# Optimization experiments

Measured on AMD Instinct MI355X. Metric: run time of the kernel, lower is better.

## Reference

```python
import jax, jax.numpy as jnp
import numpy as np

B, S_SRC, S_TGT, H, V = 32, 128, 64, 300, 32000


def setup_inputs() -> dict:
    key = jax.random.key(0)
    ks = jax.random.split(key, 16)

    def n(k, shape, scale=0.05):
        return jax.random.normal(k, shape, dtype=jnp.float32) * scale

    return {
        "x": jax.random.randint(ks[0], (B, S_SRC), 0, V),
        "y": jax.random.randint(ks[1], (B, S_TGT), 0, V),
        "h0": jax.random.normal(ks[2], (B, H), dtype=jnp.float32),  # encoder initNormState (L=1 squeezed)
        "EN": n(ks[3], (V, H)),
        "ZH": n(ks[4], (V, H)),
        "enc_Wih": n(ks[5], (H, H)),
        "enc_Whh": n(ks[6], (H, H)),
        "enc_bih": n(ks[7], (H,)),
        "enc_bhh": n(ks[8], (H,)),
        "dec_Wih": n(ks[9], (H, H)),
        "dec_Whh": n(ks[10], (H, H)),
        "dec_bih": n(ks[11], (H,)),
        "dec_bhh": n(ks[12], (H,)),
        "W_out": n(ks[13], (V, H)),
        "b_out": n(ks[14], (V,)),
    }


def reference(x, y, h0, EN, ZH, enc_Wih, enc_Whh, enc_bih, enc_bhh,
              dec_Wih, dec_Whh, dec_bih, dec_bhh, W_out, b_out):
    # ---- encoder: 1-layer tanh RNN over source embeddings ----
    xe = EN[x]  # [B, S_src, H]

    def enc_step(h, xt):  # xt: [B, H]
        h = jnp.tanh(xt @ enc_Wih.T + enc_bih + h @ enc_Whh.T + enc_bhh)
        return h, None

    c, _ = jax.lax.scan(enc_step, h0, jnp.swapaxes(xe, 0, 1))  # c: [B, H] final hidden

    # ---- decoder: original loop always feeds encoder state c (never the updated
    # hidden) to the RNNCell; with teacher forcing (start_TF_rate=1.0) every step
    # uses y_in[t], so all T steps vectorize into one batched computation. ----
    ye = ZH[y]  # [B, T, H]
    dec_state_term = c @ dec_Whh.T + dec_bhh  # [B, H], shared across all steps
    h_dec = jnp.tanh(ye @ dec_Wih.T + dec_bih + dec_state_term[:, None, :])  # [B, T, H]
    out = h_dec @ W_out.T + b_out  # [B, T, V]
    return out
```

## Files before the change

### kernel.cpp

```cpp
#include <hip/hip_runtime.h>
#include <hip/hip_bf16.h>
#include <stdint.h>

#define BB 32
#define S_SRC 128
#define S_TGT 64
#define H 300
#define VV 32000
#define M_ROWS (BB * S_TGT)
#define KP 320

#define MEGA_T 640
#define ENC_BLK 32
#define HDEC_BLK 128
#define WCVT_BLK 96

typedef __attribute__((ext_vector_type(8))) __bf16 bf16x8;
typedef __attribute__((ext_vector_type(4))) float f32x4;
typedef __attribute__((ext_vector_type(4))) unsigned short u16x4;
typedef __attribute__((ext_vector_type(2))) __fp16 f16x2;

#if defined(__has_builtin)
#if __has_builtin(__builtin_amdgcn_fdot2)
#define HAVE_FDOT2 1
#endif
#endif

__device__ inline unsigned short f2bf(float f) {
    union { float f; unsigned u; } v; v.f = f;
    unsigned r = (v.u + 0x7FFF + ((v.u >> 16) & 1)) >> 16;
    return (unsigned short)r;
}

__device__ __forceinline__ float ftanh(float x) {
    float e = __builtin_amdgcn_exp2f(x * 2.8853900817779268f);
    return 1.0f - 2.0f * __builtin_amdgcn_rcpf(e + 1.0f);
}

__device__ __forceinline__ float fdot2(f16x2 a, f16x2 b, float c) {
#ifdef HAVE_FDOT2
    return __builtin_amdgcn_fdot2(a, b, c, false);
#else
    return c + (float)a.x * (float)b.x + (float)a.y * (float)b.y;
#endif
}

__device__ __forceinline__ void gl_lds16(const void* g, void* l) {
    __builtin_amdgcn_global_load_lds(
        (const __attribute__((address_space(1))) void*)g,
        (__attribute__((address_space(3))) void*)l, 16, 0, 0);
}

__global__ void transpose4(const float* W0, const float* W1, const float* W2,
                           const float* W3, float* dst) {
    const float* srcs[4] = {W0, W1, W2, W3};
    const float* src = srcs[blockIdx.z];
    float* d = dst + (size_t)blockIdx.z * (H * H);
    __shared__ float tile[32][33];
    int j0 = blockIdx.y * 32, k0 = blockIdx.x * 32;
    for (int r = threadIdx.y; r < 32; r += blockDim.y) {
        int j = j0 + r, k = k0 + threadIdx.x;
        tile[r][threadIdx.x] = (j < H && k < H) ? src[(size_t)j * H + k] : 0.f;
    }
    __syncthreads();
    for (int r = threadIdx.y; r < 32; r += blockDim.y) {
        int k = k0 + r, j = j0 + threadIdx.x;
        if (k < H && j < H) d[(size_t)k * H + j] = tile[threadIdx.x][r];
    }
}

#define RPB 8
__global__ __launch_bounds__(192) void pproj(const int* __restrict__ x,
                                             const float* __restrict__ EN,
                                             const float* __restrict__ WihT,
                                             const float* __restrict__ bih,
                                             const float* __restrict__ bhh,
                                             float* __restrict__ P) {
    __shared__ float xe[RPB][H];
    int m0 = blockIdx.x * RPB;
    int tid = threadIdx.x;
    for (int r = 0; r < RPB; ++r) {
        int idx = x[m0 + r];
        for (int c = tid; c < H; c += 192) xe[r][c] = EN[(size_t)idx * H + c];
    }
    __syncthreads();
    if (tid < 150) {
        int j = tid * 2;
        float a0[RPB], a1[RPB];
#pragma unroll
        for (int r = 0; r < RPB; ++r) { a0[r] = 0.f; a1[r] = 0.f; }
        const float* wp = WihT + j;
        for (int k = 0; k < H; ++k) {
            float2 w = *reinterpret_cast<const float2*>(wp + (size_t)k * H);
#pragma unroll
            for (int r = 0; r < RPB; ++r) {
                float xv = xe[r][k];
                a0[r] += xv * w.x; a1[r] += xv * w.y;
            }
        }
        float b0 = bih[j] + bhh[j], b1 = bih[j + 1] + bhh[j + 1];
#pragma unroll
        for (int r = 0; r < RPB; ++r) {
            P[(size_t)(m0 + r) * H + j]     = a0[r] + b0;
            P[(size_t)(m0 + r) * H + j + 1] = a1[r] + b1;
        }
    }
}

__global__ __launch_bounds__(MEGA_T) void mega(
    const float* __restrict__ h0, const float* __restrict__ P,
    const float* __restrict__ Whh, float* __restrict__ c,
    const int* __restrict__ yv, const float* __restrict__ ZH,
    const float* __restrict__ WihT_d, const float* __restrict__ bih_d,
    float* __restrict__ t1,
    const float* __restrict__ W, unsigned short* __restrict__ Wb) {
    __shared__ union {
        __fp16 hb[2][304];
        float  ye[16][304];
    } L;
    int blk = blockIdx.x, tid = threadIdx.x;

    if (blk < ENC_BLK) {
        int b = blk;
        bool act = tid < 600;
        int j = tid >> 1, half = tid & 1;
        f16x2 w[76];
        if (act) {
            const float* wr = Whh + (size_t)j * H + half * 150;
#pragma unroll
            for (int i = 0; i < 75; ++i) {
                float2 f = *reinterpret_cast<const float2*>(wr + 2 * i);
                w[i] = __builtin_amdgcn_cvt_pkrtz(f.x, f.y);
            }
            w[75] = __builtin_amdgcn_cvt_pkrtz(0.f, 0.f);
        }
        if (act && half == 0) {
            int pos = j < 150 ? j : j + 2;
            L.hb[0][pos] = (__fp16)h0[(size_t)b * H + j];
        }
        if (tid >= 600 && tid < 608) {
            int pi = tid - 600, bufi = pi >> 2, q = pi & 3;
            int idx = (q < 2) ? (150 + q) : (302 + (q - 2));
            L.hb[bufi][idx] = (__fp16)0.f;
        }
        __syncthreads();

        const float* Pb = P + (size_t)b * S_SRC * H;
        int cur = 0;
        for (int t = 0; t < S_SRC; ++t) {
            float pv = 0.f;
            if (act && half == 0) pv = Pb[(size_t)t * H + j];
            float tot = 0.f;
            if (act) {
                float a0 = 0.f, a1 = 0.f, a2 = 0.f, a3 = 0.f;
                const uint2* hp =
                    reinterpret_cast<const uint2*>(&L.hb[cur][half * 152]);
#pragma unroll
                for (int i = 0; i < 38; i += 2) {
                    uint2 qa = hp[i];
                    uint2 qb = hp[i + 1];
                    a0 = fdot2(w[2 * i],     __builtin_bit_cast(f16x2, qa.x), a0);
                    a1 = fdot2(w[2 * i + 1], __builtin_bit_cast(f16x2, qa.y), a1);
                    a2 = fdot2(w[2 * i + 2], __builtin_bit_cast(f16x2, qb.x), a2);
                    a3 = fdot2(w[2 * i + 3], __builtin_bit_cast(f16x2, qb.y), a3);
                }
                float a = (a0 + a1) + (a2 + a3);
                tot = a + __shfl_xor(a, 1, 64);
                if (half == 0) {
                    float hv = ftanh(tot + pv);
                    int pos = j < 150 ? j : j + 2;
                    L.hb[cur ^ 1][pos] = (__fp16)hv;
                }
            }
            __syncthreads();
            cur ^= 1;
        }
        if (act && half == 0) {
            int pos = j < 150 ? j : j + 2;
            c[(size_t)b * H + j] = (float)L.hb[cur][pos];
        }
    } else if (blk < ENC_BLK + HDEC_BLK) {
        int bi = blk - ENC_BLK;
        int m0 = bi * 16;
        for (int i = tid; i < 16 * 304; i += MEGA_T) {
            int r = i / 304, cc = i - r * 304;
            L.ye[r][cc] = (cc < H) ? ZH[(size_t)yv[m0 + r] * H + cc] : 0.f;
        }
        __syncthreads();
        if (tid < 600) {
            int rg = tid / 150, jp = tid - rg * 150, j0 = 2 * jp;
            float a[4][2] = {};
            const float* wp = WihT_d + j0;
            for (int k = 0; k < H; k += 2) {
                float2 wa = *reinterpret_cast<const float2*>(wp + (size_t)k * H);
                float2 wb = *reinterpret_cast<const float2*>(wp + (size_t)(k + 1) * H);
#pragma unroll
                for (int r = 0; r < 4; ++r) {
                    float2 x = *reinterpret_cast<const float2*>(&L.ye[rg * 4 + r][k]);
                    a[r][0] += x.x * wa.x + x.y * wb.x;
                    a[r][1] += x.x * wa.y + x.y * wb.y;
                }
            }
            float b0 = bih_d[j0], b1 = bih_d[j0 + 1];
#pragma unroll
            for (int r = 0; r < 4; ++r) {
                *reinterpret_cast<float2*>(&t1[(size_t)(m0 + rg * 4 + r) * 304 + j0]) =
                    make_float2(a[r][0] + b0, a[r][1] + b1);
            }
        }
    } else if (Wb != nullptr) {
        for (int id = (blk - (ENC_BLK + HDEC_BLK)) * MEGA_T + tid; id < VV * 80;
             id += WCVT_BLK * MEGA_T) {
            int row = id / 80, cq = id - row * 80;
            int k = cq * 4;
            u16x4 o;
            if (k < H) {
                float4 f = *reinterpret_cast<const float4*>(W + (size_t)row * H + k);
                o[0] = f2bf(f.x); o[1] = f2bf(f.y); o[2] = f2bf(f.z); o[3] = f2bf(f.w);
            } else {
                o[0] = 0; o[1] = 0; o[2] = 0; o[3] = 0;
            }
            *reinterpret_cast<u16x4*>(Wb + (size_t)row * KP + k) = o;
        }
    }
}

__global__ __launch_bounds__(192) void sdec(const float* __restrict__ c,
                                            const float* __restrict__ WhhT_d,
                                            const float* __restrict__ bhh_d,
                                            float* __restrict__ s2) {
    __shared__ float cl[H];
    int b = blockIdx.x, tid = threadIdx.x;
    for (int k = tid; k < H; k += 192) cl[k] = c[(size_t)b * H + k];
    __syncthreads();
    if (tid < 150) {
        int j = tid * 2;
        float a0 = 0.f, a1 = 0.f;
        const float* wp = WhhT_d + j;
        for (int k = 0; k < H; ++k) {
            float2 w = *reinterpret_cast<const float2*>(wp + (size_t)k * H);
            a0 += cl[k] * w.x; a1 += cl[k] * w.y;
        }
        s2[(size_t)b * H + j]     = a0 + bhh_d[j];
        s2[(size_t)b * H + j + 1] = a1 + bhh_d[j + 1];
    }
}

__global__ __launch_bounds__(256) void hdec_fin(const float* __restrict__ t1,
                                                const float* __restrict__ s2,
                                                unsigned short* __restrict__ hdec) {
    int blk = blockIdx.x, tid = threadIdx.x;
    for (int i = tid; i < 8 * KP; i += 256) {
        int r = i / KP, j = i - r * KP;
        int m = blk * 8 + r, b = m >> 6;
        unsigned short v = 0;
        if (j < H)
            v = f2bf(ftanh(t1[(size_t)m * 304 + j] + s2[(size_t)b * H + j]));
        hdec[(size_t)m * KP + j] = v;
    }
}

__global__ __launch_bounds__(256) void gemm2(const unsigned short* __restrict__ A,
                                             const unsigned short* __restrict__ Wb,
                                             const float* __restrict__ bout,
                                             float* __restrict__ out) {
    __shared__ unsigned short Al[2][128 * 64];
    __shared__ unsigned short Blds[2][128 * 64];
    int tid = threadIdx.x;
    int lane = tid & 63, wv = tid >> 6;
    int wm = wv >> 1, wn = wv & 1;

    int orig = blockIdx.x;
    int wg = (orig & 7) * 500 + (orig >> 3);
    int mi = wg & 15, ni = wg >> 4;
    int m0 = mi * 128, n0 = ni * 128;

    int rowb = tid >> 3;
    int sc2 = (tid & 7) ^ (rowb & 7);

    f32x4 acc[4][4];
    f32x4 zero = {0.f, 0.f, 0.f, 0.f};
#pragma unroll
    for (int i = 0; i < 4; ++i)
#pragma unroll
        for (int j = 0; j < 4; ++j) acc[i][j] = zero;

#pragma unroll
    for (int i = 0; i < 4; ++i) {
        int row = i * 32 + rowb;
        gl_lds16(A + (size_t)(m0 + row) * KP + sc2 * 8, &Al[0][(i * 256 + tid) * 8]);
    }
#pragma unroll
    for (int i = 0; i < 4; ++i) {
        int row = i * 32 + rowb;
        gl_lds16(Wb + (size_t)(n0 + row) * KP + sc2 * 8, &Blds[0][(i * 256 + tid) * 8]);
    }

    for (int t = 0; t < 5; ++t) {
        __syncthreads();
        int buf = t & 1;
        if (t < 4) {
            int k0 = (t + 1) * 64, nb = buf ^ 1;
#pragma unroll
            for (int i = 0; i < 4; ++i) {
                int row = i * 32 + rowb;
                gl_lds16(A + (size_t)(m0 + row) * KP + k0 + sc2 * 8,
                         &Al[nb][(i * 256 + tid) * 8]);
            }
#pragma unroll
            for (int i = 0; i < 4; ++i) {
                int row = i * 32 + rowb;
                gl_lds16(Wb + (size_t)(n0 + row) * KP + k0 + sc2 * 8,
                         &Blds[nb][(i * 256 + tid) * 8]);
            }
        }
        bf16x8 af[2][4], bb[2][4];
#pragma unroll
        for (int ks = 0; ks < 2; ++ks)
#pragma unroll
            for (int i = 0; i < 4; ++i) {
                int ch = (ks * 4 + (lane >> 4)) ^ (lane & 7);
                int rowA = wm * 64 + i * 16 + (lane & 15);
                af[ks][i] = *reinterpret_cast<const bf16x8*>(&Al[buf][rowA * 64 + ch * 8]);
                int rowB = wn * 64 + i * 16 + (lane & 15);
                bb[ks][i] = *reinterpret_cast<const bf16x8*>(&Blds[buf][rowB * 64 + ch * 8]);
            }
#pragma unroll
        for (int ks = 0; ks < 2; ++ks)
#pragma unroll
            for (int i = 0; i < 4; ++i)
#pragma unroll
                for (int j = 0; j < 4; ++j)
                    acc[i][j] = __builtin_amdgcn_mfma_f32_16x16x32_bf16(
                        af[ks][i], bb[ks][j], acc[i][j], 0, 0, 0);
    }

#pragma unroll
    for (int j = 0; j < 4; ++j) {
        int col = n0 + wn * 64 + j * 16 + (lane & 15);
        float bo = bout[col];
#pragma unroll
        for (int i = 0; i < 4; ++i) {
            int rb = m0 + wm * 64 + i * 16 + (lane >> 4) * 4;
            f32x4 v = acc[i][j];
#pragma unroll
            for (int r = 0; r < 4; ++r)
                out[(size_t)(rb + r) * VV + col] = v[r] + bo;
        }
    }
}

#define LDSW 40
__global__ __launch_bounds__(256) void gemm_out(const unsigned short* __restrict__ A,
                                                const float* __restrict__ W,
                                                const float* __restrict__ bout,
                                                float* __restrict__ out) {
    __shared__ __align__(16) unsigned short Alds[128 * LDSW];
    __shared__ __align__(16) unsigned short Bl[128 * LDSW];
    int tid = threadIdx.x;
    int lane = tid & 63, wv = tid >> 6;
    int wm = wv >> 1, wn = wv & 1;
    int m0 = blockIdx.y * 128, n0 = blockIdx.x * 128;

    f32x4 acc[4][4];
    f32x4 zero = {0.f, 0.f, 0.f, 0.f};
#pragma unroll
    for (int i = 0; i < 4; ++i)
#pragma unroll
        for (int jj = 0; jj < 4; ++jj) acc[i][jj] = zero;

    for (int k0 = 0; k0 < KP; k0 += 32) {
#pragma unroll
        for (int s = 0; s < 2; ++s) {
            int slot = tid + s * 256;
            int row = slot >> 2, c16 = slot & 3;
            uint4 v = *reinterpret_cast<const uint4*>(
                &A[(size_t)(m0 + row) * KP + k0 + c16 * 8]);
            *reinterpret_cast<uint4*>(&Alds[row * LDSW + c16 * 8]) = v;
        }
#pragma unroll
        for (int s = 0; s < 2; ++s) {
            int slot = tid + s * 256;
            int row = slot >> 2, c8 = slot & 3;
            int k = k0 + c8 * 8;
            __align__(16) unsigned short tmp[8];
            if (k + 7 < H) {
                const float* src = &W[(size_t)(n0 + row) * H + k];
                float4 f0 = *reinterpret_cast<const float4*>(src);
                float4 f1 = *reinterpret_cast<const float4*>(src + 4);
                tmp[0] = f2bf(f0.x); tmp[1] = f2bf(f0.y);
                tmp[2] = f2bf(f0.z); tmp[3] = f2bf(f0.w);
                tmp[4] = f2bf(f1.x); tmp[5] = f2bf(f1.y);
                tmp[6] = f2bf(f1.z); tmp[7] = f2bf(f1.w);
            } else {
#pragma unroll
                for (int jv = 0; jv < 8; ++jv) {
                    int kk = k + jv;
                    tmp[jv] = (kk < H) ? f2bf(W[(size_t)(n0 + row) * H + kk])
                                       : (unsigned short)0;
                }
            }
            *reinterpret_cast<uint4*>(&Bl[row * LDSW + c8 * 8]) =
                *reinterpret_cast<const uint4*>(tmp);
        }
        __syncthreads();
        bf16x8 af[4], bfm[4];
#pragma unroll
        for (int i = 0; i < 4; ++i) {
            int row = wm * 64 + i * 16 + (lane & 15);
            af[i] = *reinterpret_cast<const bf16x8*>(&Alds[row * LDSW + (lane >> 4) * 8]);
        }
#pragma unroll
        for (int i = 0; i < 4; ++i) {
            int row = wn * 64 + i * 16 + (lane & 15);
            bfm[i] = *reinterpret_cast<const bf16x8*>(&Bl[row * LDSW + (lane >> 4) * 8]);
        }
#pragma unroll
        for (int i = 0; i < 4; ++i)
#pragma unroll
            for (int jj = 0; jj < 4; ++jj)
                acc[i][jj] = __builtin_amdgcn_mfma_f32_16x16x32_bf16(
                    af[i], bfm[jj], acc[i][jj], 0, 0, 0);
        __syncthreads();
    }
#pragma unroll
    for (int jj = 0; jj < 4; ++jj) {
        int col = n0 + wn * 64 + jj * 16 + (lane & 15);
        float bo = bout[col];
#pragma unroll
        for (int i = 0; i < 4; ++i) {
            int rb = m0 + wm * 64 + i * 16 + (lane >> 4) * 4;
            f32x4 v = acc[i][jj];
#pragma unroll
            for (int r = 0; r < 4; ++r)
                out[(size_t)(rb + r) * VV + col] = v[r] + bo;
        }
    }
}

extern "C" void kernel_launch(void* const* d_in, const int* in_sizes, int n_in,
                              void* d_out, int out_size, void* d_ws, size_t ws_size,
                              hipStream_t stream) {
    const int*   x       = (const int*)d_in[0];
    const int*   y       = (const int*)d_in[1];
    const float* h0      = (const float*)d_in[2];
    const float* EN      = (const float*)d_in[3];
    const float* ZH      = (const float*)d_in[4];
    const float* enc_Wih = (const float*)d_in[5];
    const float* enc_Whh = (const float*)d_in[6];
    const float* enc_bih = (const float*)d_in[7];
    const float* enc_bhh = (const float*)d_in[8];
    const float* dec_Wih = (const float*)d_in[9];
    const float* dec_Whh = (const float*)d_in[10];
    const float* dec_bih = (const float*)d_in[11];
    const float* dec_bhh = (const float*)d_in[12];
    const float* W_out   = (const float*)d_in[13];
    const float* b_out   = (const float*)d_in[14];
    float* out = (float*)d_out;
    char* base = (char*)d_ws;

    const size_t needA = 23307520, needB = 2827520;
    bool bigws = (ws_size >= needA);
    if (!bigws && ws_size < needB) return;

    float* WT = (float*)base;
    float *c_, *s2_;
    unsigned short *hdec, *Wb = nullptr;
    if (bigws) {
        Wb   = (unsigned short*)(base + 1440000);
        c_   = (float*)(base + 21920000);
        s2_  = (float*)(base + 21958400);
        hdec = (unsigned short*)(base + 21996800);
    } else {
        c_   = (float*)(base + 1440000);
        s2_  = (float*)(base + 1478400);
        hdec = (unsigned short*)(base + 1516800);
    }
    float* P  = out;
    float* t1 = out + 2000000;

    transpose4<<<dim3(10, 10, 4), dim3(32, 8), 0, stream>>>(
        enc_Wih, enc_Whh, dec_Wih, dec_Whh, WT);
    pproj<<<(BB * S_SRC) / RPB, 192, 0, stream>>>(x, EN, WT, enc_bih, enc_bhh, P);
    int mega_grid = bigws ? (ENC_BLK + HDEC_BLK + WCVT_BLK) : (ENC_BLK + HDEC_BLK);
    mega<<<mega_grid, MEGA_T, 0, stream>>>(h0, P, enc_Whh, c_, y, ZH,
                                           WT + 180000, dec_bih, t1, W_out, Wb);
    sdec<<<BB, 192, 0, stream>>>(c_, WT + 270000, dec_bhh, s2_);
    hdec_fin<<<M_ROWS / 8, 256, 0, stream>>>(t1, s2_, hdec);
    if (bigws) {
        gemm2<<<4000, 256, 0, stream>>>(hdec, Wb, b_out, out);
    } else {
        gemm_out<<<dim3(VV / 128, M_ROWS / 128), 256, 0, stream>>>(hdec, W_out, b_out, out);
    }
}
```

Measured before the change: 256.5 us.

## Fuse decoder state projection into encoder blocks and enlarge output GEMM tiles

The decoder state term (c @ dec_Whh^T + bhh) is now computed inside the encoder blocks of the mega kernel directly from the final hidden state in LDS. This drops the separate sdec launch and the c round trip, and lets transpose handle only two matrices. The output GEMM moves from 128x128 tiles with 256 threads to 256x256 tiles with 512 threads and 2 blocks/SM, raising data reuse per tile. The cost is more accumulator registers, more LDS, and fewer blocks (1000) to fill the GPU.

```diff
diff --git a/kernel.cpp b/kernel.cpp
--- a/kernel.cpp
+++ b/kernel.cpp
@@ -51,9 +51,8 @@
         (__attribute__((address_space(3))) void*)l, 16, 0, 0);
 }
 
-__global__ void transpose4(const float* W0, const float* W1, const float* W2,
-                           const float* W3, float* dst) {
-    const float* srcs[4] = {W0, W1, W2, W3};
+__global__ void transpose2(const float* W0, const float* W1, float* dst) {
+    const float* srcs[2] = {W0, W1};
     const float* src = srcs[blockIdx.z];
     float* d = dst + (size_t)blockIdx.z * (H * H);
     __shared__ float tile[32][33];
@@ -109,7 +108,9 @@
 
 __global__ __launch_bounds__(MEGA_T) void mega(
     const float* __restrict__ h0, const float* __restrict__ P,
-    const float* __restrict__ Whh, float* __restrict__ c,
+    const float* __restrict__ Whh,
+    const float* __restrict__ dWhh, const float* __restrict__ dbhh,
+    float* __restrict__ s2,
     const int* __restrict__ yv, const float* __restrict__ ZH,
     const float* __restrict__ WihT_d, const float* __restrict__ bih_d,
     float* __restrict__ t1,
@@ -150,7 +151,6 @@
         for (int t = 0; t < S_SRC; ++t) {
             float pv = 0.f;
             if (act && half == 0) pv = Pb[(size_t)t * H + j];
-            float tot = 0.f;
             if (act) {
                 float a0 = 0.f, a1 = 0.f, a2 = 0.f, a3 = 0.f;
                 const uint2* hp =
@@ -165,7 +165,7 @@
                     a3 = fdot2(w[2 * i + 3], __builtin_bit_cast(f16x2, qb.y), a3);
                 }
                 float a = (a0 + a1) + (a2 + a3);
-                tot = a + __shfl_xor(a, 1, 64);
+                float tot = a + __shfl_xor(a, 1, 64);
                 if (half == 0) {
                     float hv = ftanh(tot + pv);
                     int pos = j < 150 ? j : j + 2;
@@ -175,9 +175,28 @@
             __syncthreads();
             cur ^= 1;
         }
-        if (act && half == 0) {
-            int pos = j < 150 ? j : j + 2;
-            c[(size_t)b * H + j] = (float)L.hb[cur][pos];
+        if (act) {
+            const float* wr = dWhh + (size_t)j * H + half * 150;
+            const uint2* hp = reinterpret_cast<const uint2*>(&L.hb[cur][half * 152]);
+            float a0 = 0.f, a1 = 0.f;
+#pragma unroll
+            for (int i = 0; i < 37; ++i) {
+                uint2 q = hp[i];
+                f16x2 hA = __builtin_bit_cast(f16x2, q.x);
+                f16x2 hB = __builtin_bit_cast(f16x2, q.y);
+                float4 wf = *reinterpret_cast<const float4*>(wr + 4 * i);
+                a0 += wf.x * (float)hA.x + wf.y * (float)hA.y;
+                a1 += wf.z * (float)hB.x + wf.w * (float)hB.y;
+            }
+            {
+                f16x2 hA = __builtin_bit_cast(f16x2,
+                    reinterpret_cast<const uint*>(&L.hb[cur][half * 152])[74]);
+                float2 wf = *reinterpret_cast<const float2*>(wr + 148);
+                a0 += wf.x * (float)hA.x + wf.y * (float)hA.y;
+            }
+            float a = a0 + a1;
+            float tot = a + __shfl_xor(a, 1, 64);
+            if (half == 0) s2[(size_t)b * H + j] = tot + dbhh[j];
         }
     } else if (blk < ENC_BLK + HDEC_BLK) {
         int bi = blk - ENC_BLK;
@@ -225,27 +244,6 @@
     }
 }
 
-__global__ __launch_bounds__(192) void sdec(const float* __restrict__ c,
-                                            const float* __restrict__ WhhT_d,
-                                            const float* __restrict__ bhh_d,
-                                            float* __restrict__ s2) {
-    __shared__ float cl[H];
-    int b = blockIdx.x, tid = threadIdx.x;
-    for (int k = tid; k < H; k += 192) cl[k] = c[(size_t)b * H + k];
-    __syncthreads();
-    if (tid < 150) {
-        int j = tid * 2;
-        float a0 = 0.f, a1 = 0.f;
-        const float* wp = WhhT_d + j;
-        for (int k = 0; k < H; ++k) {
-            float2 w = *reinterpret_cast<const float2*>(wp + (size_t)k * H);
-            a0 += cl[k] * w.x; a1 += cl[k] * w.y;
-        }
-        s2[(size_t)b * H + j]     = a0 + bhh_d[j];
-        s2[(size_t)b * H + j + 1] = a1 + bhh_d[j + 1];
-    }
-}
-
 __global__ __launch_bounds__(256) void hdec_fin(const float* __restrict__ t1,
                                                 const float* __restrict__ s2,
                                                 unsigned short* __restrict__ hdec) {
@@ -260,40 +258,40 @@
     }
 }
 
-__global__ __launch_bounds__(256) void gemm2(const unsigned short* __restrict__ A,
-                                             const unsigned short* __restrict__ Wb,
-                                             const float* __restrict__ bout,
-                                             float* __restrict__ out) {
-    __shared__ unsigned short Al[2][128 * 64];
-    __shared__ unsigned short Blds[2][128 * 64];
+__global__ __launch_bounds__(512, 2) void gemm3(const unsigned short* __restrict__ A,
+                                                const unsigned short* __restrict__ Wb,
+                                                const float* __restrict__ bout,
+                                                float* __restrict__ out) {
+    __shared__ unsigned short Al[2][256 * 64];
+    __shared__ unsigned short Bl[2][256 * 64];
     int tid = threadIdx.x;
     int lane = tid & 63, wv = tid >> 6;
-    int wm = wv >> 1, wn = wv & 1;
+    int wm = wv >> 2, wn = wv & 3;
 
     int orig = blockIdx.x;
-    int wg = (orig & 7) * 500 + (orig >> 3);
-    int mi = wg & 15, ni = wg >> 4;
-    int m0 = mi * 128, n0 = ni * 128;
+    int wg = (orig & 7) * 125 + (orig >> 3);
+    int mi = wg & 7, ni = wg >> 3;
+    int m0 = mi * 256, n0 = ni * 256;
 
     int rowb = tid >> 3;
-    int sc2 = (tid & 7) ^ (rowb & 7);
-
-    f32x4 acc[4][4];
+    int sc = (tid & 7) ^ (rowb & 7);
+
+    f32x4 acc[8][4];
     f32x4 zero = {0.f, 0.f, 0.f, 0.f};
 #pragma unroll
-    for (int i = 0; i < 4; ++i)
+    for (int i = 0; i < 8; ++i)
 #pragma unroll
         for (int j = 0; j < 4; ++j) acc[i][j] = zero;
 
 #pragma unroll
     for (int i = 0; i < 4; ++i) {
-        int row = i * 32 + rowb;
-        gl_lds16(A + (size_t)(m0 + row) * KP + sc2 * 8, &Al[0][(i * 256 + tid) * 8]);
+        int row = i * 64 + rowb;
+        gl_lds16(A + (size_t)(m0 + row) * KP + sc * 8, &Al[0][(i * 512 + tid) * 8]);
     }
 #pragma unroll
     for (int i = 0; i < 4; ++i) {
-        int row = i * 32 + rowb;
-        gl_lds16(Wb + (size_t)(n0 + row) * KP + sc2 * 8, &Blds[0][(i * 256 + tid) * 8]);
+        int row = i * 64 + rowb;
+        gl_lds16(Wb + (size_t)(n0 + row) * KP + sc * 8, &Bl[0][(i * 512 + tid) * 8]);
     }
 
     for (int t = 0; t < 5; ++t) {
@@ -303,36 +301,38 @@
             int k0 = (t + 1) * 64, nb = buf ^ 1;
 #pragma unroll
             for (int i = 0; i < 4; ++i) {
-                int row = i * 32 + rowb;
-                gl_lds16(A + (size_t)(m0 + row) * KP + k0 + sc2 * 8,
-                         &Al[nb][(i * 256 + tid) * 8]);
+                int row = i * 64 + rowb;
+                gl_lds16(A + (size_t)(m0 + row) * KP + k0 + sc * 8,
+                         &Al[nb][(i * 512 + tid) * 8]);
             }
 #pragma unroll
             for (int i = 0; i < 4; ++i) {
-                int row = i * 32 + rowb;
-                gl_lds16(Wb + (size_t)(n0 + row) * KP + k0 + sc2 * 8,
-                         &Blds[nb][(i * 256 + tid) * 8]);
-            }
-        }
-        bf16x8 af[2][4], bb[2][4];
-#pragma unroll
-        for (int ks = 0; ks < 2; ++ks)
-#pragma unroll
-            for (int i = 0; i < 4; ++i) {
-                int ch = (ks * 4 + (lane >> 4)) ^ (lane & 7);
-                int rowA = wm * 64 + i * 16 + (lane & 15);
-                af[ks][i] = *reinterpret_cast<const bf16x8*>(&Al[buf][rowA * 64 + ch * 8]);
-                int rowB = wn * 64 + i * 16 + (lane & 15);
-                bb[ks][i] = *reinterpret_cast<const bf16x8*>(&Blds[buf][rowB * 64 + ch * 8]);
-            }
-#pragma unroll
-        for (int ks = 0; ks < 2; ++ks)
-#pragma unroll
-            for (int i = 0; i < 4; ++i)
+                int row = i * 64 + rowb;
+                gl_lds16(Wb + (size_t)(n0 + row) * KP + k0 + sc * 8,
+                         &Bl[nb][(i * 512 + tid) * 8]);
+            }
+        }
+#pragma unroll
+        for (int ks = 0; ks < 2; ++ks) {
+            bf16x8 af[8], bb[4];
+            int slot = (ks * 4 + (lane >> 4)) ^ (lane & 7);
+#pragma unroll
+            for (int i = 0; i < 8; ++i) {
+                int row = wm * 128 + i * 16 + (lane & 15);
+                af[i] = *reinterpret_cast<const bf16x8*>(&Al[buf][row * 64 + slot * 8]);
+            }
+#pragma unroll
+            for (int j = 0; j < 4; ++j) {
+                int row = wn * 64 + j * 16 + (lane & 15);
+                bb[j] = *reinterpret_cast<const bf16x8*>(&Bl[buf][row * 64 + slot * 8]);
+            }
+#pragma unroll
+            for (int i = 0; i < 8; ++i)
 #pragma unroll
                 for (int j = 0; j < 4; ++j)
                     acc[i][j] = __builtin_amdgcn_mfma_f32_16x16x32_bf16(
-                        af[ks][i], bb[ks][j], acc[i][j], 0, 0, 0);
+                        af[i], bb[j], acc[i][j], 0, 0, 0);
+        }
     }
 
 #pragma unroll
@@ -340,8 +340,8 @@
         int col = n0 + wn * 64 + j * 16 + (lane & 15);
         float bo = bout[col];
 #pragma unroll
-        for (int i = 0; i < 4; ++i) {
-            int rb = m0 + wm * 64 + i * 16 + (lane >> 4) * 4;
+        for (int i = 0; i < 8; ++i) {
+            int rb = m0 + wm * 128 + i * 16 + (lane >> 4) * 4;
             f32x4 v = acc[i][j];
 #pragma unroll
             for (int r = 0; r < 4; ++r)
@@ -459,36 +459,33 @@
     float* out = (float*)d_out;
     char* base = (char*)d_ws;
 
-    const size_t needA = 23307520, needB = 2827520;
+    const size_t needA = 22549120, needB = 2069120;
     bool bigws = (ws_size >= needA);
     if (!bigws && ws_size < needB) return;
 
     float* WT = (float*)base;
-    float *c_, *s2_;
+    float *s2_;
     unsigned short *hdec, *Wb = nullptr;
     if (bigws) {
-        Wb   = (unsigned short*)(base + 1440000);
-        c_   = (float*)(base + 21920000);
-        s2_  = (float*)(base + 21958400);
-        hdec = (unsigned short*)(base + 21996800);
+        Wb   = (unsigned short*)(base + 720000);
+        s2_  = (float*)(base + 21200000);
+        hdec = (unsigned short*)(base + 21238400);
     } else {
-        c_   = (float*)(base + 1440000);
-        s2_  = (float*)(base + 1478400);
-        hdec = (unsigned short*)(base + 1516800);
+        s2_  = (float*)(base + 720000);
+        hdec = (unsigned short*)(base + 758400);
     }
     float* P  = out;
     float* t1 = out + 2000000;
 
-    transpose4<<<dim3(10, 10, 4), dim3(32, 8), 0, stream>>>(
-        enc_Wih, enc_Whh, dec_Wih, dec_Whh, WT);
+    transpose2<<<dim3(10, 10, 2), dim3(32, 8), 0, stream>>>(enc_Wih, dec_Wih, WT);
     pproj<<<(BB * S_SRC) / RPB, 192, 0, stream>>>(x, EN, WT, enc_bih, enc_bhh, P);
     int mega_grid = bigws ? (ENC_BLK + HDEC_BLK + WCVT_BLK) : (ENC_BLK + HDEC_BLK);
-    mega<<<mega_grid, MEGA_T, 0, stream>>>(h0, P, enc_Whh, c_, y, ZH,
-                                           WT + 180000, dec_bih, t1, W_out, Wb);
-    sdec<<<BB, 192, 0, stream>>>(c_, WT + 270000, dec_bhh, s2_);
+    mega<<<mega_grid, MEGA_T, 0, stream>>>(h0, P, enc_Whh, dec_Whh, dec_bhh, s2_,
+                                           y, ZH, WT + 90000, dec_bih, t1,
+                                           W_out, Wb);
     hdec_fin<<<M_ROWS / 8, 256, 0, stream>>>(t1, s2_, hdec);
     if (bigws) {
-        gemm2<<<4000, 256, 0, stream>>>(hdec, Wb, b_out, out);
+        gemm3<<<1000, 512, 0, stream>>>(hdec, Wb, b_out, out);
     } else {
         gemm_out<<<dim3(VV / 128, M_ROWS / 128), 256, 0, stream>>>(hdec, W_out, b_out, out);
     }
```

Result: slower. 264.6 us (+3.1%).
